# Performance work log

Measured on AMD Instinct MI355X. Metric: run time of the kernel, lower is better.

The kernel has to match this reference:

```python
import jax, jax.numpy as jnp
import numpy as np

N = 100000      # nodes
E = 1600000     # graph edges (avg degree 16)
Q = 1000000     # query edges to score
IN, HID, OUT = 128, 128, 64


def setup_inputs() -> dict:
    key = jax.random.key(0)
    ks = jax.random.split(key, 7)
    feat = jax.random.normal(ks[0], (N, IN), dtype=jnp.float32)
    edge_src = jax.random.randint(ks[1], (E,), 0, N, dtype=jnp.int32)
    edge_dst = jax.random.randint(ks[2], (E,), 0, N, dtype=jnp.int32)
    src = jax.random.randint(ks[3], (Q,), 0, N, dtype=jnp.int32)
    dst = jax.random.randint(ks[4], (Q,), 0, N, dtype=jnp.int32)
    W1 = jax.random.normal(ks[5], (IN, HID), dtype=jnp.float32) / np.sqrt(IN).astype(np.float32)
    b1 = jnp.zeros((HID,), jnp.float32)
    W2 = jax.random.normal(ks[6], (HID, OUT), dtype=jnp.float32) / np.sqrt(HID).astype(np.float32)
    b2 = jnp.zeros((OUT,), jnp.float32)
    return {"feat": feat, "edge_src": edge_src, "edge_dst": edge_dst,
            "src": src, "dst": dst, "W1": W1, "b1": b1, "W2": W2, "b2": b2}


def _graph_conv(h, W, b, edge_src, edge_dst, out_norm, in_norm):
    """DGL GraphConv(norm='both'): D_out^{-1/2} -> aggregate -> D_in^{-1/2}, W, b.
    DGL applies W before aggregation when in_feats > out_feats (same math)."""
    n = h.shape[0]
    h = h * out_norm[:, None]
    if h.shape[1] > W.shape[1]:
        h = h @ W
        agg = jax.ops.segment_sum(h[edge_src], edge_dst, num_segments=n)
    else:
        agg = jax.ops.segment_sum(h[edge_src], edge_dst, num_segments=n)
        agg = agg @ W
    return agg * in_norm[:, None] + b


def reference(feat, edge_src, edge_dst, src, dst, W1, b1, W2, b2):
    n = feat.shape[0]
    ones = jnp.ones((edge_src.shape[0],), feat.dtype)
    out_deg = jax.ops.segment_sum(ones, edge_src, num_segments=n)
    in_deg = jax.ops.segment_sum(ones, edge_dst, num_segments=n)
    out_norm = jnp.maximum(out_deg, 1.0) ** -0.5
    in_norm = jnp.maximum(in_deg, 1.0) ** -0.5

    h = _graph_conv(feat, W1, b1, edge_src, edge_dst, out_norm, in_norm)
    h = jax.nn.relu(h)  # dropout is identity at inference
    h = _graph_conv(h, W2, b2, edge_src, edge_dst, out_norm, in_norm)

    edge_scores = jnp.sum(h[src] * h[dst], axis=-1)
    return jax.nn.sigmoid(edge_scores)
```

## Files before the change

kernel.cpp:

```cpp
#include <hip/hip_runtime.h>
#include <math.h>

static inline size_t align256(size_t x) { return (x + 255) & ~(size_t)255; }

typedef __attribute__((ext_vector_type(8))) short bf16x8;
typedef __attribute__((ext_vector_type(4))) float f32x4;
typedef __attribute__((ext_vector_type(2))) float f32x2;
typedef __attribute__((ext_vector_type(2))) _Float16 half2_t;

__device__ inline float bfLo(unsigned int u) {
  union { unsigned int i; float f; } v; v.i = u << 16; return v.f;
}
__device__ inline float bfHi(unsigned int u) {
  union { unsigned int i; float f; } v; v.i = u & 0xffff0000u; return v.f;
}
__device__ inline unsigned short f2bf(float f) {
  union { float f; unsigned int i; } v; v.f = f;
  unsigned int r = v.i + 0x7FFF + ((v.i >> 16) & 1);
  return (unsigned short)(r >> 16);
}
__device__ inline unsigned int packbf(float lo, float hi) {
  return ((unsigned int)f2bf(hi) << 16) | f2bf(lo);
}
__device__ inline unsigned int packh(float lo, float hi) {
  union { _Float16 h[2]; unsigned int u; } v;
  v.h[0] = (_Float16)lo; v.h[1] = (_Float16)hi;
  return v.u;
}

__device__ inline f32x2 f8lo(unsigned int u) {
  return __builtin_amdgcn_cvt_pk_f32_fp8(u, false);
}
__device__ inline f32x2 f8hi(unsigned int u) {
  return __builtin_amdgcn_cvt_pk_f32_fp8(u, true);
}
__device__ inline unsigned char f2f8(float f) {
  unsigned int v = (unsigned int)__builtin_amdgcn_cvt_pk_fp8_f32(f, f, 0, false);
  return (unsigned char)(v & 0xffu);
}
__device__ inline unsigned int pack4f8(float a, float b, float c, float d) {
  unsigned int v = (unsigned int)__builtin_amdgcn_cvt_pk_fp8_f32(a, b, 0, false);
  v = (unsigned int)__builtin_amdgcn_cvt_pk_fp8_f32(c, d, (int)v, true);
  return v;
}

__global__ __launch_bounds__(256) void k_coarse_count(const int* __restrict__ esrc,
                                                      const int* __restrict__ edst,
                                                      int E, int chunk, int NB, int G,
                                                      int* __restrict__ blkD,
                                                      int* __restrict__ blkS,
                                                      const float* __restrict__ W1,
                                                      const float* __restrict__ W2,
                                                      unsigned short* __restrict__ W1t,
                                                      unsigned short* __restrict__ W2t) {
  __shared__ int hD[512], hS[512];
  int blk = blockIdx.x, tid = threadIdx.x;
  int t = blk * 256 + tid;
  if (t < 128 * 128) {
    int nn = t >> 7, kk = t & 127;
    W1t[t] = f2bf(W1[kk * 128 + nn]);
  }
  if (t < 64 * 128) {
    int nn = t >> 7, kk = t & 127;
    W2t[t] = f2bf(W2[kk * 64 + nn]);
  }
  for (int i = tid; i < NB; i += 256) { hD[i] = 0; hS[i] = 0; }
  __syncthreads();
  int s0 = blk * chunk, s1 = min(E, s0 + chunk);
  for (int e = s0 + tid; e < s1; e += 256) {
    atomicAdd(&hD[edst[e] >> 8], 1);
    atomicAdd(&hS[esrc[e] >> 8], 1);
  }
  __syncthreads();
  for (int i = tid; i < NB; i += 256) {
    blkD[i * G + blk] = hD[i];
    blkS[i * G + blk] = hS[i];
  }
}

__global__ __launch_bounds__(256) void k_scan1(const int* __restrict__ in,
                                               int* __restrict__ out,
                                               int* __restrict__ bsums, int n) {
  __shared__ int s[256];
  int tid = threadIdx.x, gid = blockIdx.x * 256 + tid;
  int v = (gid < n) ? in[gid] : 0;
  s[tid] = v; __syncthreads();
  for (int o = 1; o < 256; o <<= 1) {
    int t = (tid >= o) ? s[tid - o] : 0;
    __syncthreads();
    s[tid] += t;
    __syncthreads();
  }
  if (gid < n) out[gid] = s[tid] - v;
  if (tid == 255) bsums[blockIdx.x] = s[255];
}

__global__ __launch_bounds__(512) void k_scan2(int* __restrict__ bsums, int nb) {
  __shared__ int s[512];
  int tid = threadIdx.x;
  int* base = bsums + blockIdx.x * nb;
  int v = (tid < nb) ? base[tid] : 0;
  s[tid] = v; __syncthreads();
  for (int o = 1; o < 512; o <<= 1) {
    int t = (tid >= o) ? s[tid - o] : 0;
    __syncthreads();
    s[tid] += t;
    __syncthreads();
  }
  if (tid < nb) base[tid] = s[tid] - v;
}

__global__ __launch_bounds__(256) void k_coarse_scatter(const int* __restrict__ esrc,
                                                        const int* __restrict__ edst,
                                                        int E, int chunk, int NB, int G,
                                                        const int* __restrict__ scD,
                                                        const int* __restrict__ scS,
                                                        const int* __restrict__ bsums,
                                                        unsigned int* __restrict__ pairs,
                                                        unsigned int* __restrict__ keys) {
  __shared__ int cD[512], cS[512];
  int blk = blockIdx.x, tid = threadIdx.x;
  for (int i = tid; i < NB; i += 256) {
    cD[i] = scD[i * G + blk] + bsums[i];
    cS[i] = scS[i * G + blk] + bsums[NB + i];
  }
  __syncthreads();
  int s0 = blk * chunk, s1 = min(E, s0 + chunk);
  for (int e = s0 + tid; e < s1; e += 256) {
    int s = esrc[e], d = edst[e];
    int pd = atomicAdd(&cD[d >> 8], 1);
    pairs[pd] = ((unsigned)s << 8) | ((unsigned)d & 255u);
    int ps = atomicAdd(&cS[s >> 8], 1);
    keys[ps] = (unsigned)s;
  }
}

__global__ __launch_bounds__(256) void k_fine(const unsigned int* __restrict__ pairs,
                                              const unsigned int* __restrict__ keys,
                                              const int* __restrict__ scD,
                                              const int* __restrict__ scS,
                                              const int* __restrict__ bsums,
                                              int G, int E, int N, int NB,
                                              int* __restrict__ cntIn,
                                              float* __restrict__ normIn,
                                              int* __restrict__ offs,
                                              int* __restrict__ csr,
                                              float* __restrict__ normOut) {
  __shared__ int hist[256], scn[256], cur[256];
  int tid = threadIdx.x;
  if (blockIdx.x >= (unsigned)NB) {
    int b = blockIdx.x - NB;
    int bstart = scS[b * G] + bsums[NB + b];
    int bend = (b + 1 < NB) ? scS[(b + 1) * G] + bsums[NB + b + 1] : E;
    hist[tid] = 0;
    __syncthreads();
    for (int e = bstart + tid; e < bend; e += 256)
      atomicAdd(&hist[keys[e] & 255u], 1);
    __syncthreads();
    int node = b * 256 + tid;
    if (node < N) normOut[node] = rsqrtf((float)max(hist[tid], 1));
    return;
  }
  int b = blockIdx.x;
  int bstart = scD[b * G] + bsums[b];
  int bend = (b + 1 < NB) ? scD[(b + 1) * G] + bsums[b + 1] : E;
  hist[tid] = 0;
  __syncthreads();
  for (int e = bstart + tid; e < bend; e += 256)
    atomicAdd(&hist[pairs[e] & 255u], 1);
  __syncthreads();
  int v = hist[tid];
  scn[tid] = v;
  __syncthreads();
  for (int o = 1; o < 256; o <<= 1) {
    int t = (tid >= o) ? scn[tid - o] : 0;
    __syncthreads();
    scn[tid] += t;
    __syncthreads();
  }
  int excl = scn[tid] - v;
  cur[tid] = excl;
  int node = b * 256 + tid;
  if (node < N) {
    cntIn[node] = v;
    normIn[node] = rsqrtf((float)max(v, 1));
    offs[node] = bstart + excl;
  }
  __syncthreads();
  for (int e = bstart + tid; e < bend; e += 256) {
    unsigned int u = pairs[e];
    int p = bstart + atomicAdd(&cur[u & 255u], 1);
    csr[p] = (int)(u >> 8);
  }
}

template <int C, typename TA, bool OF8>
__global__ __launch_bounds__(256) void k_mgemm(const TA* __restrict__ A,
                                               const float* __restrict__ scale,
                                               const unsigned short* __restrict__ Wt,
                                               unsigned short* __restrict__ out, int n) {
  constexpr int KP = 136;
  constexpr int NCH = C / 16;
  __shared__ __align__(16) unsigned short Al[64 * KP];
  __shared__ __align__(16) unsigned short Wl[C * KP];
  int tid = threadIdx.x;
  int r0 = blockIdx.x * 64;

  {
    const uint4* Wg = (const uint4*)Wt;
    uint4* Wd = (uint4*)Wl;
    for (int idx = tid; idx < C * 16; idx += 256) {
      int row = idx >> 4, seg = idx & 15;
      Wd[row * 17 + seg] = Wg[idx];
    }
  }
  {
    int seg = tid & 7;
    for (int it = 0; it < 2; ++it) {
      int row = (tid >> 3) + it * 32;
      int g = r0 + row;
      float v[16];
      if (g < n) {
        float sc = scale[g];
        if constexpr (sizeof(TA) == 4) {
          const float4* Ag = (const float4*)((const float*)A + (size_t)g * 128);
#pragma unroll
          for (int j = 0; j < 4; ++j) {
            float4 f = Ag[seg * 4 + j];
            v[j * 4 + 0] = f.x * sc; v[j * 4 + 1] = f.y * sc;
            v[j * 4 + 2] = f.z * sc; v[j * 4 + 3] = f.w * sc;
          }
        } else {
          const uint4* Ag = (const uint4*)((const unsigned short*)A + (size_t)g * 128);
#pragma unroll
          for (int j = 0; j < 2; ++j) {
            uint4 u = Ag[seg * 2 + j];
            v[j * 8 + 0] = bfLo(u.x) * sc; v[j * 8 + 1] = bfHi(u.x) * sc;
            v[j * 8 + 2] = bfLo(u.y) * sc; v[j * 8 + 3] = bfHi(u.y) * sc;
            v[j * 8 + 4] = bfLo(u.z) * sc; v[j * 8 + 5] = bfHi(u.z) * sc;
            v[j * 8 + 6] = bfLo(u.w) * sc; v[j * 8 + 7] = bfHi(u.w) * sc;
          }
        }
      } else {
#pragma unroll
        for (int j = 0; j < 16; ++j) v[j] = 0.f;
      }
      uint4* dst = (uint4*)(Al + row * KP + seg * 16);
      dst[0] = make_uint4(packbf(v[0], v[1]), packbf(v[2], v[3]),
                          packbf(v[4], v[5]), packbf(v[6], v[7]));
      dst[1] = make_uint4(packbf(v[8], v[9]), packbf(v[10], v[11]),
                          packbf(v[12], v[13]), packbf(v[14], v[15]));
    }
  }
  __syncthreads();

  int lane = tid & 63;
  int w = tid >> 6;
  int quad = lane >> 4, m16 = lane & 15;
  f32x4 acc[NCH];
#pragma unroll
  for (int c = 0; c < NCH; ++c) acc[c] = (f32x4){0.f, 0.f, 0.f, 0.f};

#pragma unroll
  for (int kc = 0; kc < 4; ++kc) {
    int ko = kc * 32 + quad * 8;
    bf16x8 a = *(const bf16x8*)(Al + (w * 16 + m16) * KP + ko);
#pragma unroll
    for (int c = 0; c < NCH; ++c) {
      bf16x8 b = *(const bf16x8*)(Wl + (c * 16 + m16) * KP + ko);
      acc[c] = __builtin_amdgcn_mfma_f32_16x16x32_bf16(a, b, acc[c], 0, 0, 0);
    }
  }

  if constexpr (OF8) {
    unsigned char* o8 = (unsigned char*)out;
#pragma unroll
    for (int c = 0; c < NCH; ++c)
#pragma unroll
      for (int r = 0; r < 4; ++r) {
        int g = r0 + w * 16 + quad * 4 + r;
        if (g < n) o8[(size_t)g * C + c * 16 + m16] = f2f8(acc[c][r]);
      }
  } else {
#pragma unroll
    for (int c = 0; c < NCH; ++c)
#pragma unroll
      for (int r = 0; r < 4; ++r) {
        int g = r0 + w * 16 + quad * 4 + r;
        if (g < n) out[(size_t)g * C + c * 16 + m16] = f2bf(acc[c][r]);
      }
  }
}

__global__ __launch_bounds__(256) void k_agg128f8_relu(const unsigned char* __restrict__ X,
                                                       const int* __restrict__ csr,
                                                       const int* __restrict__ offs,
                                                       const int* __restrict__ cnt,
                                                       const float* __restrict__ norm,
                                                       const float* __restrict__ bias,
                                                       unsigned short* __restrict__ H, int n) {
  int wid = blockIdx.x * 4 + (threadIdx.x >> 6);
  if (wid >= n) return;
  int lane = threadIdx.x & 63;
  int sub = lane & 15;
  int grp = lane >> 4;
  int start = offs[wid], m = cnt[wid];
  const int* p = csr + start;
  const uint2* Xv = (const uint2*)X;
  f32x2 a0 = {0.f, 0.f}, a1 = {0.f, 0.f}, a2 = {0.f, 0.f}, a3 = {0.f, 0.f};
  for (int c0 = 0; c0 < m; c0 += 64) {
    int take = min(64, m - c0);
    int iv = p[c0 + ((lane < take) ? lane : take - 1)];
    int full = take & ~15;
    int e = 0;
    for (; e < full; e += 16) {
      uint2 uu[4];
#pragma unroll
      for (int j = 0; j < 4; ++j) {
        int ss = __shfl(iv, e + j * 4 + grp);
        uu[j] = Xv[(size_t)ss * 16 + sub];
      }
#pragma unroll
      for (int j = 0; j < 4; ++j) {
        a0 += f8lo(uu[j].x); a1 += f8hi(uu[j].x);
        a2 += f8lo(uu[j].y); a3 += f8hi(uu[j].y);
      }
    }
    if (e < take) {
      uint2 uu[4];
      int vm[4];
#pragma unroll
      for (int j = 0; j < 4; ++j) {
        int idx = e + j * 4 + grp;
        vm[j] = (idx < take);
        int ss = __shfl(iv, vm[j] ? idx : take - 1);
        uu[j] = Xv[(size_t)ss * 16 + sub];
      }
#pragma unroll
      for (int j = 0; j < 4; ++j) {
        unsigned ux = vm[j] ? uu[j].x : 0u;
        unsigned uy = vm[j] ? uu[j].y : 0u;
        a0 += f8lo(ux); a1 += f8hi(ux);
        a2 += f8lo(uy); a3 += f8hi(uy);
      }
    }
  }
  float a[8] = {a0.x, a0.y, a1.x, a1.y, a2.x, a2.y, a3.x, a3.y};
#pragma unroll
  for (int k = 0; k < 8; ++k) {
    a[k] += __shfl_xor(a[k], 16);
    a[k] += __shfl_xor(a[k], 32);
  }
  float nm = norm[wid];
  const float4* bv = (const float4*)bias;
  float4 b0 = bv[sub * 2], b1 = bv[sub * 2 + 1];
  if (grp == 0) {
    float o0 = fmaxf(a[0] * nm + b0.x, 0.f);
    float o1 = fmaxf(a[1] * nm + b0.y, 0.f);
    float o2 = fmaxf(a[2] * nm + b0.z, 0.f);
    float o3 = fmaxf(a[3] * nm + b0.w, 0.f);
    float o4 = fmaxf(a[4] * nm + b1.x, 0.f);
    float o5 = fmaxf(a[5] * nm + b1.y, 0.f);
    float o6 = fmaxf(a[6] * nm + b1.z, 0.f);
    float o7 = fmaxf(a[7] * nm + b1.w, 0.f);
    uint4 o = make_uint4(packbf(o0, o1), packbf(o2, o3),
                         packbf(o4, o5), packbf(o6, o7));
    ((uint4*)H)[(size_t)wid * 16 + sub] = o;
  }
}

__global__ __launch_bounds__(256) void k_agg64f8(const unsigned char* __restrict__ X,
                                                 const int* __restrict__ csr,
                                                 const int* __restrict__ offs,
                                                 const int* __restrict__ cnt,
                                                 const float* __restrict__ norm,
                                                 const float* __restrict__ bias,
                                                 unsigned char* __restrict__ H, int n) {
  int wid = blockIdx.x * 4 + (threadIdx.x >> 6);
  if (wid >= n) return;
  int lane = threadIdx.x & 63;
  int sub = lane & 15;
  int grp = lane >> 4;
  int start = offs[wid], m = cnt[wid];
  const int* p = csr + start;
  const unsigned* Xv = (const unsigned*)X;
  f32x2 a0 = {0.f, 0.f}, a1 = {0.f, 0.f};
  for (int c0 = 0; c0 < m; c0 += 64) {
    int take = min(64, m - c0);
    int iv = p[c0 + ((lane < take) ? lane : take - 1)];
    int full = take & ~15;
    int e = 0;
    for (; e < full; e += 16) {
      unsigned uu[4];
#pragma unroll
      for (int j = 0; j < 4; ++j) {
        int ss = __shfl(iv, e + j * 4 + grp);
        uu[j] = Xv[(size_t)ss * 16 + sub];
      }
#pragma unroll
      for (int j = 0; j < 4; ++j) {
        a0 += f8lo(uu[j]); a1 += f8hi(uu[j]);
      }
    }
    if (e < take) {
      unsigned uu[4];
      int vm[4];
#pragma unroll
      for (int j = 0; j < 4; ++j) {
        int idx = e + j * 4 + grp;
        vm[j] = (idx < take);
        int ss = __shfl(iv, vm[j] ? idx : take - 1);
        uu[j] = Xv[(size_t)ss * 16 + sub];
      }
#pragma unroll
      for (int j = 0; j < 4; ++j) {
        unsigned u = vm[j] ? uu[j] : 0u;
        a0 += f8lo(u); a1 += f8hi(u);
      }
    }
  }
  float a[4] = {a0.x, a0.y, a1.x, a1.y};
#pragma unroll
  for (int k = 0; k < 4; ++k) {
    a[k] += __shfl_xor(a[k], 16);
    a[k] += __shfl_xor(a[k], 32);
  }
  if (grp == 0) {
    float nm = norm[wid];
    const float4* bv = (const float4*)bias;
    float4 b0 = bv[sub];
    unsigned w0 = pack4f8(a[0] * nm + b0.x, a[1] * nm + b0.y,
                          a[2] * nm + b0.z, a[3] * nm + b0.w);
    ((unsigned*)H)[(size_t)wid * 16 + sub] = w0;
  }
}

__global__ __launch_bounds__(256) void k_score(const unsigned char* __restrict__ H,
                                               const int* __restrict__ qs,
                                               const int* __restrict__ qd,
                                               float* __restrict__ out, int q, int qStride) {
  int t = blockIdx.x * 256 + threadIdx.x;
  int sub = t & 7;
  int q0 = t >> 3;
  const uint2* Hv = (const uint2*)H;
  int qi[4];
  bool has[4];
  uint2 A[4], B[4];
#pragma unroll
  for (int i = 0; i < 4; ++i) {
    qi[i] = q0 + i * qStride;
    has[i] = (qi[i] < q);
  }
#pragma unroll
  for (int i = 0; i < 4; ++i) {
    if (has[i]) {
      A[i] = Hv[(size_t)qs[qi[i]] * 8 + sub];
      B[i] = Hv[(size_t)qd[qi[i]] * 8 + sub];
    }
  }
  float p[4] = {0.f, 0.f, 0.f, 0.f};
#pragma unroll
  for (int i = 0; i < 4; ++i) {
    if (has[i]) {
      f32x2 acc = f8lo(A[i].x) * f8lo(B[i].x);
      acc += f8hi(A[i].x) * f8hi(B[i].x);
      acc += f8lo(A[i].y) * f8lo(B[i].y);
      acc += f8hi(A[i].y) * f8hi(B[i].y);
      p[i] = acc.x + acc.y;
    }
  }
#pragma unroll
  for (int i = 0; i < 4; ++i) {
    p[i] += __shfl_xor(p[i], 1);
    p[i] += __shfl_xor(p[i], 2);
    p[i] += __shfl_xor(p[i], 4);
  }
  if (sub == 0) {
#pragma unroll
    for (int i = 0; i < 4; ++i)
      if (has[i]) out[qi[i]] = 1.f / (1.f + expf(-p[i]));
  }
}

extern "C" void kernel_launch(void* const* d_in, const int* in_sizes, int n_in,
                              void* d_out, int out_size, void* d_ws, size_t ws_size,
                              hipStream_t stream) {
  const float* feat = (const float*)d_in[0];
  const int* esrc   = (const int*)d_in[1];
  const int* edst   = (const int*)d_in[2];
  const int* qsrc   = (const int*)d_in[3];
  const int* qdst   = (const int*)d_in[4];
  const float* W1   = (const float*)d_in[5];
  const float* b1   = (const float*)d_in[6];
  const float* W2   = (const float*)d_in[7];
  const float* b2   = (const float*)d_in[8];
  float* out = (float*)d_out;

  const int N = in_sizes[0] / 128;
  const int E = in_sizes[1];
  const int Q = in_sizes[3];

  const int G = 256;
  const int NB = (N + 255) >> 8;
  const int chunk = (E + G - 1) / G;
  const int lenS = NB * G;
  const int gScan = lenS / 256;

  char* w = (char*)d_ws;
  size_t o = 0;
  unsigned char* bufA = (unsigned char*)(w + o); o += align256((size_t)N * 128);
  unsigned short* bufH1 = (unsigned short*)(w + o); o += align256((size_t)N * 128 * 2);
  unsigned char* bufH2 = (unsigned char*)(w + o); o += align256((size_t)N * 64);
  int* cntIn = (int*)(w + o);       o += align256((size_t)N * 4);
  float* normOut = (float*)(w + o); o += align256((size_t)N * 4);
  float* normIn = (float*)(w + o);  o += align256((size_t)N * 4);
  int* offs = (int*)(w + o);        o += align256((size_t)N * 4);
  int* blk = (int*)(w + o);         o += align256((size_t)lenS * 8);
  int* sc = (int*)(w + o);          o += align256((size_t)lenS * 8);
  int* bsums = (int*)(w + o);       o += align256((size_t)8192);
  unsigned short* W1t = (unsigned short*)(w + o); o += align256((size_t)128 * 128 * 2);
  unsigned short* W2t = (unsigned short*)(w + o); o += align256((size_t)64 * 128 * 2);
  unsigned int* pairs = (unsigned int*)(w + o); o += align256((size_t)E * 4);
  unsigned int* keys = (unsigned int*)(w + o); o += align256((size_t)E * 4);
  int* csr = (int*)(w + o);         o += align256((size_t)E * 4);

  int* blkD = blk;        int* blkS = blk + lenS;
  int* scD = sc;          int* scS = sc + lenS;

  k_coarse_count<<<G, 256, 0, stream>>>(esrc, edst, E, chunk, NB, G, blkD, blkS,
                                        W1, W2, W1t, W2t);
  k_scan1<<<2 * gScan, 256, 0, stream>>>(blk, sc, bsums, 2 * lenS);
  k_scan2<<<2, 512, 0, stream>>>(bsums, gScan);
  k_coarse_scatter<<<G, 256, 0, stream>>>(esrc, edst, E, chunk, NB, G, scD, scS,
                                          bsums, pairs, keys);
  k_fine<<<2 * NB, 256, 0, stream>>>(pairs, keys, scD, scS, bsums, G, E, N, NB,
                                     cntIn, normIn, offs, csr, normOut);

  const int gRows = (N + 63) / 64;
  k_mgemm<128, float, true><<<gRows, 256, 0, stream>>>(feat, normOut, W1t,
                                                       (unsigned short*)bufA, N);
  k_agg128f8_relu<<<(N + 3) / 4, 256, 0, stream>>>(bufA, csr, offs, cntIn, normIn,
                                                   b1, bufH1, N);
  k_mgemm<64, unsigned short, true><<<gRows, 256, 0, stream>>>(bufH1, normOut, W2t,
                                                               (unsigned short*)bufA, N);
  k_agg64f8<<<(N + 3) / 4, 256, 0, stream>>>(bufA, csr, offs, cntIn, normIn, b2,
                                             bufH2, N);
  const int qQuarter = (Q + 3) / 4;
  k_score<<<((qQuarter * 8) + 255) / 256, 256, 0, stream>>>(bufH2, qsrc, qdst, out,
                                                            Q, qQuarter);
}
```

Measured before the change: 299.6 us.

## Compute out-degree with global atomics instead of a second bucket sort

```diff
diff --git a/kernel.cpp b/kernel.cpp
--- a/kernel.cpp
+++ b/kernel.cpp
@@ -22,11 +22,6 @@
 __device__ inline unsigned int packbf(float lo, float hi) {
   return ((unsigned int)f2bf(hi) << 16) | f2bf(lo);
 }
-__device__ inline unsigned int packh(float lo, float hi) {
-  union { _Float16 h[2]; unsigned int u; } v;
-  v.h[0] = (_Float16)lo; v.h[1] = (_Float16)hi;
-  return v.u;
-}
 
 __device__ inline f32x2 f8lo(unsigned int u) {
   return __builtin_amdgcn_cvt_pk_f32_fp8(u, false);
@@ -48,12 +43,12 @@
                                                       const int* __restrict__ edst,
                                                       int E, int chunk, int NB, int G,
                                                       int* __restrict__ blkD,
-                                                      int* __restrict__ blkS,
+                                                      int* __restrict__ outdeg,
                                                       const float* __restrict__ W1,
                                                       const float* __restrict__ W2,
                                                       unsigned short* __restrict__ W1t,
                                                       unsigned short* __restrict__ W2t) {
-  __shared__ int hD[512], hS[512];
+  __shared__ int hD[512];
   int blk = blockIdx.x, tid = threadIdx.x;
   int t = blk * 256 + tid;
   if (t < 128 * 128) {
@@ -64,25 +59,26 @@
     int nn = t >> 7, kk = t & 127;
     W2t[t] = f2bf(W2[kk * 64 + nn]);
   }
-  for (int i = tid; i < NB; i += 256) { hD[i] = 0; hS[i] = 0; }
+  for (int i = tid; i < NB; i += 256) hD[i] = 0;
   __syncthreads();
   int s0 = blk * chunk, s1 = min(E, s0 + chunk);
   for (int e = s0 + tid; e < s1; e += 256) {
     atomicAdd(&hD[edst[e] >> 8], 1);
-    atomicAdd(&hS[esrc[e] >> 8], 1);
-  }
-  __syncthreads();
-  for (int i = tid; i < NB; i += 256) {
+    atomicAdd(&outdeg[esrc[e]], 1);
+  }
+  __syncthreads();
+  for (int i = tid; i < NB; i += 256)
     blkD[i * G + blk] = hD[i];
-    blkS[i * G + blk] = hS[i];
-  }
 }
 
 __global__ __launch_bounds__(256) void k_scan1(const int* __restrict__ in,
                                                int* __restrict__ out,
-                                               int* __restrict__ bsums, int n) {
+                                               int* __restrict__ bsums, int n,
+                                               const int* __restrict__ outdeg,
+                                               float* __restrict__ normOut, int N) {
   __shared__ int s[256];
   int tid = threadIdx.x, gid = blockIdx.x * 256 + tid;
+  if (gid < N) normOut[gid] = rsqrtf((float)max(outdeg[gid], 1));
   int v = (gid < n) ? in[gid] : 0;
   s[tid] = v; __syncthreads();
   for (int o = 1; o < 256; o <<= 1) {
@@ -98,8 +94,7 @@
 __global__ __launch_bounds__(512) void k_scan2(int* __restrict__ bsums, int nb) {
   __shared__ int s[512];
   int tid = threadIdx.x;
-  int* base = bsums + blockIdx.x * nb;
-  int v = (tid < nb) ? base[tid] : 0;
+  int v = (tid < nb) ? bsums[tid] : 0;
   s[tid] = v; __syncthreads();
   for (int o = 1; o < 512; o <<= 1) {
     int t = (tid >= o) ? s[tid - o] : 0;
@@ -107,60 +102,38 @@
     s[tid] += t;
     __syncthreads();
   }
-  if (tid < nb) base[tid] = s[tid] - v;
+  if (tid < nb) bsums[tid] = s[tid] - v;
 }
 
 __global__ __launch_bounds__(256) void k_coarse_scatter(const int* __restrict__ esrc,
                                                         const int* __restrict__ edst,
                                                         int E, int chunk, int NB, int G,
                                                         const int* __restrict__ scD,
-                                                        const int* __restrict__ scS,
                                                         const int* __restrict__ bsums,
-                                                        unsigned int* __restrict__ pairs,
-                                                        unsigned int* __restrict__ keys) {
-  __shared__ int cD[512], cS[512];
+                                                        unsigned int* __restrict__ pairs) {
+  __shared__ int cD[512];
   int blk = blockIdx.x, tid = threadIdx.x;
-  for (int i = tid; i < NB; i += 256) {
+  for (int i = tid; i < NB; i += 256)
     cD[i] = scD[i * G + blk] + bsums[i];
-    cS[i] = scS[i * G + blk] + bsums[NB + i];
-  }
   __syncthreads();
   int s0 = blk * chunk, s1 = min(E, s0 + chunk);
   for (int e = s0 + tid; e < s1; e += 256) {
     int s = esrc[e], d = edst[e];
     int pd = atomicAdd(&cD[d >> 8], 1);
     pairs[pd] = ((unsigned)s << 8) | ((unsigned)d & 255u);
-    int ps = atomicAdd(&cS[s >> 8], 1);
-    keys[ps] = (unsigned)s;
   }
 }
 
 __global__ __launch_bounds__(256) void k_fine(const unsigned int* __restrict__ pairs,
-                                              const unsigned int* __restrict__ keys,
                                               const int* __restrict__ scD,
-                                              const int* __restrict__ scS,
                                               const int* __restrict__ bsums,
                                               int G, int E, int N, int NB,
                                               int* __restrict__ cntIn,
                                               float* __restrict__ normIn,
                                               int* __restrict__ offs,
-                                              int* __restrict__ csr,
-                                              float* __restrict__ normOut) {
+                                              int* __restrict__ csr) {
   __shared__ int hist[256], scn[256], cur[256];
   int tid = threadIdx.x;
-  if (blockIdx.x >= (unsigned)NB) {
-    int b = blockIdx.x - NB;
-    int bstart = scS[b * G] + bsums[NB + b];
-    int bend = (b + 1 < NB) ? scS[(b + 1) * G] + bsums[NB + b + 1] : E;
-    hist[tid] = 0;
-    __syncthreads();
-    for (int e = bstart + tid; e < bend; e += 256)
-      atomicAdd(&hist[keys[e] & 255u], 1);
-    __syncthreads();
-    int node = b * 256 + tid;
-    if (node < N) normOut[node] = rsqrtf((float)max(hist[tid], 1));
-    return;
-  }
   int b = blockIdx.x;
   int bstart = scD[b * G] + bsums[b];
   int bend = (b + 1 < NB) ? scD[(b + 1) * G] + bsums[b + 1] : E;
@@ -515,26 +488,23 @@
   float* normOut = (float*)(w + o); o += align256((size_t)N * 4);
   float* normIn = (float*)(w + o);  o += align256((size_t)N * 4);
   int* offs = (int*)(w + o);        o += align256((size_t)N * 4);
-  int* blk = (int*)(w + o);         o += align256((size_t)lenS * 8);
-  int* sc = (int*)(w + o);          o += align256((size_t)lenS * 8);
-  int* bsums = (int*)(w + o);       o += align256((size_t)8192);
+  int* outdeg = (int*)(w + o);      o += align256((size_t)N * 4);
+  int* blk = (int*)(w + o);         o += align256((size_t)lenS * 4);
+  int* sc = (int*)(w + o);          o += align256((size_t)lenS * 4);
+  int* bsums = (int*)(w + o);       o += align256((size_t)4096);
   unsigned short* W1t = (unsigned short*)(w + o); o += align256((size_t)128 * 128 * 2);
   unsigned short* W2t = (unsigned short*)(w + o); o += align256((size_t)64 * 128 * 2);
   unsigned int* pairs = (unsigned int*)(w + o); o += align256((size_t)E * 4);
-  unsigned int* keys = (unsigned int*)(w + o); o += align256((size_t)E * 4);
   int* csr = (int*)(w + o);         o += align256((size_t)E * 4);
 
-  int* blkD = blk;        int* blkS = blk + lenS;
-  int* scD = sc;          int* scS = sc + lenS;
-
-  k_coarse_count<<<G, 256, 0, stream>>>(esrc, edst, E, chunk, NB, G, blkD, blkS,
+  hipMemsetAsync(outdeg, 0, (size_t)N * 4, stream);
+  k_coarse_count<<<G, 256, 0, stream>>>(esrc, edst, E, chunk, NB, G, blk, outdeg,
                                         W1, W2, W1t, W2t);
-  k_scan1<<<2 * gScan, 256, 0, stream>>>(blk, sc, bsums, 2 * lenS);
-  k_scan2<<<2, 512, 0, stream>>>(bsums, gScan);
-  k_coarse_scatter<<<G, 256, 0, stream>>>(esrc, edst, E, chunk, NB, G, scD, scS,
-                                          bsums, pairs, keys);
-  k_fine<<<2 * NB, 256, 0, stream>>>(pairs, keys, scD, scS, bsums, G, E, N, NB,
-                                     cntIn, normIn, offs, csr, normOut);
+  k_scan1<<<gScan, 256, 0, stream>>>(blk, sc, bsums, lenS, outdeg, normOut, N);
+  k_scan2<<<1, 512, 0, stream>>>(bsums, gScan);
+  k_coarse_scatter<<<G, 256, 0, stream>>>(esrc, edst, E, chunk, NB, G, sc, bsums, pairs);
+  k_fine<<<NB, 256, 0, stream>>>(pairs, sc, bsums, G, E, N, NB,
+                                 cntIn, normIn, offs, csr);
 
   const int gRows = (N + 63) / 64;
   k_mgemm<128, float, true><<<gRows, 256, 0, stream>>>(feat, normOut, W1t,
```

Result: slower. 333.8 us (+11.4%).
